# Performance work log

Hardware: AMD Instinct MI355X
Metric: run time of the kernel (lower is better)

## Reference

```python
import jax, jax.numpy as jnp
import numpy as np

N = 10000      # nodes
E = 320000     # edges (avg degree 32)
IN = 512       # in_channels
OUT = 128      # out_channels
H = 4          # in_head
C1 = 2 * OUT   # per-head hidden channels of conv1 (256)
NEG_SLOPE = 0.2


def setup_inputs() -> dict:
    key = jax.random.key(0)
    ks = jax.random.split(key, 12)
    x = jax.random.normal(ks[0], (N, IN), dtype=jnp.float32)
    edge_index = jax.random.randint(ks[1], (2, E), 0, N, dtype=jnp.int64)
    def glorot(k, shape):
        lim = np.sqrt(6.0 / (shape[0] + shape[-1])).astype(np.float32)
        return jax.random.uniform(k, shape, jnp.float32, -lim, lim)
    # conv1: GATv2Conv(IN -> C1 per head, heads=H)
    Wl1 = glorot(ks[2], (IN, H * C1))
    Wr1 = glorot(ks[3], (IN, H * C1))
    att1 = glorot(ks[4], (H, C1))
    b1 = jnp.zeros((H * C1,), jnp.float32)
    # conv2: GATv2Conv(H*C1 -> OUT, heads=1)
    Wl2 = glorot(ks[5], (H * C1, OUT))
    Wr2 = glorot(ks[6], (H * C1, OUT))
    att2 = glorot(ks[7], (1, OUT))
    b2 = jnp.zeros((OUT,), jnp.float32)
    return {"x": x, "edge_index": edge_index, "Wl1": Wl1, "Wr1": Wr1,
            "att1": att1, "b1": b1, "Wl2": Wl2, "Wr2": Wr2,
            "att2": att2, "b2": b2}


def gatv2_conv(x, src, dst, Wl, Wr, att, b, heads, ch):
    # x: [N, F_in]; src/dst: [E] (message src -> dst, softmax over dst)
    n = x.shape[0]
    xl = (x @ Wl).reshape(n, heads, ch)   # source-side projection
    xr = (x @ Wr).reshape(n, heads, ch)   # target-side projection
    # per-edge GATv2 score: att . LeakyReLU(xl_j + xr_i)   [E, H]
    e = jax.nn.leaky_relu(xl[src] + xr[dst], NEG_SLOPE)    # [E, H, C]
    s = jnp.einsum('ehc,hc->eh', e, att)                   # [E, H]
    # segment softmax over incoming edges of each dst node
    smax = jax.lax.stop_gradient(jax.ops.segment_max(s, dst, num_segments=n))
    ex = jnp.exp(s - smax[dst])
    denom = jax.ops.segment_sum(ex, dst, num_segments=n)
    alpha = ex / denom[dst]                                # [E, H]
    # weighted scatter-add of source messages
    out = jax.ops.segment_sum(alpha[:, :, None] * xl[src], dst, num_segments=n)
    return out.reshape(n, heads * ch) + b                  # concat heads + bias


def reference(x, edge_index, Wl1, Wr1, att1, b1, Wl2, Wr2, att2, b2):
    src, dst = edge_index[0], edge_index[1]
    h = gatv2_conv(x, src, dst, Wl1, Wr1, att1, b1, H, C1)
    h = jax.nn.relu(h)                                     # [N, H*C1]
    out = gatv2_conv(h, src, dst, Wl2, Wr2, att2, b2, 1, OUT)
    return out                                             # [N, OUT]
```

## Files before the change

kernel.cpp:

```cpp
#include <hip/hip_runtime.h>
#include <cfloat>

#define N_NODES 10000
#define N_EDGES 320000
#define IN_F    512
#define F1      1024
#define OUT_F   128
#define NEG     0.2f
#define BUCKET  128

typedef __attribute__((ext_vector_type(8))) short bf16x8;
typedef __attribute__((ext_vector_type(4))) float f32x4;
typedef __attribute__((ext_vector_type(2))) float f32x2;
typedef __attribute__((ext_vector_type(4))) unsigned int u32x4;

__device__ __forceinline__ float lrelu(float v) { return fmaxf(v, NEG * v); }

__device__ __forceinline__ unsigned short f2bf(float f) {
    unsigned u = __float_as_uint(f);
    u += 0x7fff + ((u >> 16) & 1);
    return (unsigned short)(u >> 16);
}
__device__ __forceinline__ float bf2f(unsigned short h) {
    return __uint_as_float(((unsigned)h) << 16);
}
__device__ __forceinline__ void u2f2(unsigned u, float& e0, float& e1) {
    e0 = __uint_as_float(u << 16);
    e1 = __uint_as_float(u & 0xffff0000u);
}

__device__ __forceinline__ float rsum16(float x) {
    x += __int_as_float(__builtin_amdgcn_update_dpp(0, __float_as_int(x), 0x121, 0xF, 0xF, false));
    x += __int_as_float(__builtin_amdgcn_update_dpp(0, __float_as_int(x), 0x122, 0xF, 0xF, false));
    x += __int_as_float(__builtin_amdgcn_update_dpp(0, __float_as_int(x), 0x124, 0xF, 0xF, false));
    x += __int_as_float(__builtin_amdgcn_update_dpp(0, __float_as_int(x), 0x128, 0xF, 0xF, false));
    return x;
}

__device__ __forceinline__ void gld_lds16(const void* g, void* l) {
    __builtin_amdgcn_global_load_lds(
        (const __attribute__((address_space(1))) unsigned int*)g,
        (__attribute__((address_space(3))) unsigned int*)l, 16, 0, 0);
}

#define PB_X  2500
#define PB_S  3750
#define PB_W1 4774
#define PB_END 5030

__device__ __forceinline__ void wt_body(const float* __restrict__ Wa,
                                        const float* __restrict__ Wb,
                                        unsigned short* __restrict__ tbf,
                                        int K, int NS, int n0, int k0, int t,
                                        float (*tile)[33]) {
    int j = t & 31;
    const float* W = (n0 < NS) ? Wa : Wb;
    int nb = (n0 < NS) ? n0 : n0 - NS;
#pragma unroll
    for (int r = 0; r < 4; ++r) {
        int kl = (t >> 5) + r * 8;
        tile[kl][j] = W[(size_t)(k0 + kl) * NS + nb + j];
    }
    __syncthreads();
#pragma unroll
    for (int r = 0; r < 4; ++r) {
        int nl = (t >> 5) + r * 8;
        tbf[(size_t)(n0 + nl) * K + k0 + j] = f2bf(tile[j][nl]);
    }
}

__global__ __launch_bounds__(256) void k_prep(const float* __restrict__ x,
                                              unsigned short* __restrict__ xbf,
                                              const int* __restrict__ ei,
                                              int* __restrict__ cnt,
                                              int* __restrict__ esrc,
                                              const float* __restrict__ Wl1,
                                              const float* __restrict__ Wr1,
                                              unsigned short* __restrict__ w1bf,
                                              const float* __restrict__ Wl2,
                                              const float* __restrict__ Wr2,
                                              unsigned short* __restrict__ w2bf) {
    __shared__ float tile[32][33];
    int bid = blockIdx.x, t = threadIdx.x;
    if (bid < PB_X) {
        int i = bid * 2048 + t * 8;
        f32x4 v0 = __builtin_nontemporal_load((const f32x4*)(x + i));
        f32x4 v1 = __builtin_nontemporal_load((const f32x4*)(x + i + 4));
        ushort4 h0, h1;
        h0.x = f2bf(v0.x); h0.y = f2bf(v0.y); h0.z = f2bf(v0.z); h0.w = f2bf(v0.w);
        h1.x = f2bf(v1.x); h1.y = f2bf(v1.y); h1.z = f2bf(v1.z); h1.w = f2bf(v1.w);
        *(ushort4*)(xbf + i) = h0;
        *(ushort4*)(xbf + i + 4) = h1;
    } else if (bid < PB_S) {
        int e = (bid - PB_X) * 256 + t;
        if (e < N_EDGES) {
            int d = ei[N_EDGES + e];
            int pos = atomicAdd(&cnt[d], 1);
            if (pos < BUCKET) esrc[(size_t)d * BUCKET + pos] = ei[e];
        }
    } else if (bid < PB_W1) {
        int local = bid - PB_S;
        wt_body(Wl1, Wr1, w1bf, IN_F, F1, (local & 63) * 32, (local >> 6) * 32, t, tile);
    } else {
        int local = bid - PB_W1;
        wt_body(Wl2, Wr2, w2bf, F1, OUT_F, (local & 7) * 32, (local >> 3) * 32, t, tile);
    }
}

template<int BM, int BN> struct GemmSmem {
    union {
        struct { short As[2 * BM * 32]; short Bs[2 * BN * 32]; } st;
        unsigned short ct[BM * (BN + 8)];
    };
};

template<int BM, int BN, int WR, int WC>
__global__ __launch_bounds__(256) void gemm_mfma(
        const unsigned short* __restrict__ A,
        const unsigned short* __restrict__ B,
        unsigned short* __restrict__ Cl, unsigned short* __restrict__ Cr,
        int M, int K, int NSPLIT, int ym,
        const int* __restrict__ cnt, int* __restrict__ esrc) {
    constexpr int NI = BM / (16 * WR);
    constexpr int NJ = BN / (16 * WC);
    __shared__ __align__(16) GemmSmem<BM, BN> sm;
    int t = threadIdx.x;
    int lane = t & 63, w = t >> 6;

    if ((int)blockIdx.y >= ym) {
        int nd = ((blockIdx.y - ym) * gridDim.x + blockIdx.x) * 4 + w;
        if (nd < N_NODES) {
            int deg = min(cnt[nd], 64);
            int p0 = nd * BUCKET;
            int v = (lane < deg) ? esrc[p0 + lane] : 0x7fffffff;
#pragma unroll
            for (int k = 2; k <= 64; k <<= 1) {
#pragma unroll
                for (int j = k >> 1; j > 0; j >>= 1) {
                    int other = __shfl_xor(v, j);
                    bool dir = ((lane & k) == 0);
                    bool lower = ((lane & j) == 0);
                    int mn = min(v, other), mx = max(v, other);
                    v = (lower == dir) ? mn : mx;
                }
            }
            if (lane < deg) esrc[p0 + lane] = v;
        }
        return;
    }

    int row0 = blockIdx.y * BM;
    int n0 = blockIdx.x * BN;
    int wr0 = (w / WC) * (NI * 16);
    int wc0 = (w % WC) * (NJ * 16);
    int q = lane >> 4, md = lane & 15;
    int srow = t >> 2;
    int skoff = (t & 3) * 8;

    f32x4 acc[NI][NJ];
#pragma unroll
    for (int i = 0; i < NI; ++i)
#pragma unroll
        for (int j = 0; j < NJ; ++j)
#pragma unroll
            for (int r = 0; r < 4; ++r) acc[i][j][r] = 0.f;

    for (int k0 = 0; k0 < K; k0 += 64) {
        __syncthreads();
#pragma unroll
        for (int pane = 0; pane < 2; ++pane)
#pragma unroll
            for (int is = 0; is < BM / 64; ++is) {
                int gr = row0 + is * 64 + srow;
                if (gr < M)
                    gld_lds16(A + (size_t)gr * K + k0 + pane * 32 + skoff,
                              &sm.st.As[pane * BM * 32 + (is * 64 + w * 16) * 32]);
            }
#pragma unroll
        for (int pane = 0; pane < 2; ++pane)
#pragma unroll
            for (int is = 0; is < BN / 64; ++is) {
                int gn = n0 + is * 64 + srow;
                gld_lds16(B + (size_t)gn * K + k0 + pane * 32 + skoff,
                          &sm.st.Bs[pane * BN * 32 + (is * 64 + w * 16) * 32]);
            }
        __syncthreads();

#pragma unroll
        for (int kk = 0; kk < 2; ++kk) {
            bf16x8 av[NI], bv[NJ];
#pragma unroll
            for (int i = 0; i < NI; ++i)
                av[i] = *(const bf16x8*)&sm.st.As[kk * BM * 32 + (wr0 + i * 16 + md) * 32 + q * 8];
#pragma unroll
            for (int j = 0; j < NJ; ++j)
                bv[j] = *(const bf16x8*)&sm.st.Bs[kk * BN * 32 + (wc0 + j * 16 + md) * 32 + q * 8];
#pragma unroll
            for (int i = 0; i < NI; ++i)
#pragma unroll
                for (int j = 0; j < NJ; ++j)
                    acc[i][j] = __builtin_amdgcn_mfma_f32_16x16x32_bf16(av[i], bv[j], acc[i][j], 0, 0, 0);
        }
    }

    __syncthreads();
#pragma unroll
    for (int i = 0; i < NI; ++i)
#pragma unroll
        for (int j = 0; j < NJ; ++j)
#pragma unroll
            for (int r = 0; r < 4; ++r)
                sm.ct[(wr0 + i * 16 + q * 4 + r) * (BN + 8) + wc0 + j * 16 + md] =
                    f2bf(acc[i][j][r]);
    __syncthreads();
    unsigned short* C = (n0 < NSPLIT) ? Cl : Cr;
    int cc0 = (n0 < NSPLIT) ? n0 : n0 - NSPLIT;
    constexpr int SEGS = BN / 8;
    for (int idx = t; idx < BM * SEGS; idx += 256) {
        int row = idx / SEGS, seg = idx % SEGS;
        if (row0 + row < M) {
            bf16x8 val = *(const bf16x8*)&sm.ct[row * (BN + 8) + seg * 8];
            *(bf16x8*)(C + (size_t)(row0 + row) * NSPLIT + cc0 + seg * 8) = val;
        }
    }
}

__global__ __launch_bounds__(256) void k_fused1(const unsigned short* __restrict__ xlbf,
                                                const unsigned short* __restrict__ xrbf,
                                                const int* __restrict__ cnt,
                                                const int* __restrict__ esrc,
                                                const float* __restrict__ att,
                                                const float* __restrict__ bias,
                                                unsigned short* __restrict__ hb) {
    int t = threadIdx.x;
    int w = t >> 6, lane = t & 63;
    int ni = w >> 1;
    int ww = w & 1;
    int nd = blockIdx.x * 2 + ni;
    int head = lane >> 4, sub = lane & 15;
    int ch = head * 256 + sub * 16;

    __shared__ float slx[4][4];
    __shared__ float4 sacc4[2][4][64];

    float4 r0, r1, r2, r3;
    {
        const u32x4* prx = (const u32x4*)(xrbf + (size_t)nd * F1 + ch);
        u32x4 xa = __builtin_nontemporal_load(prx);
        u32x4 xb = __builtin_nontemporal_load(prx + 1);
        u2f2(xa.x, r0.x, r0.y); u2f2(xa.y, r0.z, r0.w);
        u2f2(xa.z, r1.x, r1.y); u2f2(xa.w, r1.z, r1.w);
        u2f2(xb.x, r2.x, r2.y); u2f2(xb.y, r2.z, r2.w);
        u2f2(xb.z, r3.x, r3.y); u2f2(xb.w, r3.z, r3.w);
    }
    const float4* pa = (const float4*)(att + ch);
    float4 a0 = pa[0], a1 = pa[1], a2 = pa[2], a3 = pa[3];

    int deg = min(cnt[nd], BUCKET);
    int p0 = nd * BUCKET;
    int dege = min(deg, 64);
    int bkt = (lane < dege) ? esrc[p0 + lane] : 0;

    float l = 0.f;
    float4 acc0 = make_float4(0.f, 0.f, 0.f, 0.f);
    float4 acc1 = acc0, acc2 = acc0, acc3 = acc0;

    auto edge_body = [&](uint4 ca, uint4 cb) {
        float4 c0, c1, c2, c3;
        u2f2(ca.x, c0.x, c0.y); u2f2(ca.y, c0.z, c0.w);
        u2f2(ca.z, c1.x, c1.y); u2f2(ca.w, c1.z, c1.w);
        u2f2(cb.x, c2.x, c2.y); u2f2(cb.y, c2.z, c2.w);
        u2f2(cb.z, c3.x, c3.y); u2f2(cb.w, c3.z, c3.w);
        float u;
        float sl0, sa0, sl1, sa1, sl2, sa2, sl3, sa3;
        u = c0.x + r0.x; sl0 = a0.x * u;           sa0 = a0.x * fabsf(u);
        u = c0.y + r0.y; sl0 = fmaf(a0.y, u, sl0); sa0 = fmaf(a0.y, fabsf(u), sa0);
        u = c0.z + r0.z; sl0 = fmaf(a0.z, u, sl0); sa0 = fmaf(a0.z, fabsf(u), sa0);
        u = c0.w + r0.w; sl0 = fmaf(a0.w, u, sl0); sa0 = fmaf(a0.w, fabsf(u), sa0);
        u = c1.x + r1.x; sl1 = a1.x * u;           sa1 = a1.x * fabsf(u);
        u = c1.y + r1.y; sl1 = fmaf(a1.y, u, sl1); sa1 = fmaf(a1.y, fabsf(u), sa1);
        u = c1.z + r1.z; sl1 = fmaf(a1.z, u, sl1); sa1 = fmaf(a1.z, fabsf(u), sa1);
        u = c1.w + r1.w; sl1 = fmaf(a1.w, u, sl1); sa1 = fmaf(a1.w, fabsf(u), sa1);
        u = c2.x + r2.x; sl2 = a2.x * u;           sa2 = a2.x * fabsf(u);
        u = c2.y + r2.y; sl2 = fmaf(a2.y, u, sl2); sa2 = fmaf(a2.y, fabsf(u), sa2);
        u = c2.z + r2.z; sl2 = fmaf(a2.z, u, sl2); sa2 = fmaf(a2.z, fabsf(u), sa2);
        u = c2.w + r2.w; sl2 = fmaf(a2.w, u, sl2); sa2 = fmaf(a2.w, fabsf(u), sa2);
        u = c3.x + r3.x; sl3 = a3.x * u;           sa3 = a3.x * fabsf(u);
        u = c3.y + r3.y; sl3 = fmaf(a3.y, u, sl3); sa3 = fmaf(a3.y, fabsf(u), sa3);
        u = c3.z + r3.z; sl3 = fmaf(a3.z, u, sl3); sa3 = fmaf(a3.z, fabsf(u), sa3);
        u = c3.w + r3.w; sl3 = fmaf(a3.w, u, sl3); sa3 = fmaf(a3.w, fabsf(u), sa3);
        float sl = (sl0 + sl1) + (sl2 + sl3);
        float sa = (sa0 + sa1) + (sa2 + sa3);
        float s = rsum16(fmaf(0.6f, sl, 0.4f * sa));
        s = fminf(fmaxf(s, -60.f), 60.f);
        float al = __expf(s);
        l += al;
        acc0.x = fmaf(al, c0.x, acc0.x);
        acc0.y = fmaf(al, c0.y, acc0.y);
        acc0.z = fmaf(al, c0.z, acc0.z);
        acc0.w = fmaf(al, c0.w, acc0.w);
        acc1.x = fmaf(al, c1.x, acc1.x);
        acc1.y = fmaf(al, c1.y, acc1.y);
        acc1.z = fmaf(al, c1.z, acc1.z);
        acc1.w = fmaf(al, c1.w, acc1.w);
        acc2.x = fmaf(al, c2.x, acc2.x);
        acc2.y = fmaf(al, c2.y, acc2.y);
        acc2.z = fmaf(al, c2.z, acc2.z);
        acc2.w = fmaf(al, c2.w, acc2.w);
        acc3.x = fmaf(al, c3.x, acc3.x);
        acc3.y = fmaf(al, c3.y, acc3.y);
        acc3.z = fmaf(al, c3.z, acc3.z);
        acc3.w = fmaf(al, c3.w, acc3.w);
    };

    int idx = ww;
    uint4 ua, ub;
    if (idx < dege) {
        int sn = __shfl(bkt, idx);
        const uint4* pv = (const uint4*)(xlbf + (size_t)sn * F1 + ch);
        ua = pv[0]; ub = pv[1];
    }
    for (; idx < dege; idx += 2) {
        uint4 ca = ua, cb = ub;
        int nidx = idx + 2;
        if (nidx < dege) {
            int sn = __shfl(bkt, nidx);
            const uint4* pv = (const uint4*)(xlbf + (size_t)sn * F1 + ch);
            ua = pv[0]; ub = pv[1];
        }
        edge_body(ca, cb);
    }
    for (int p = p0 + 64 + ww; p < p0 + deg; p += 2) {
        const uint4* pv = (const uint4*)(xlbf + (size_t)esrc[p] * F1 + ch);
        edge_body(pv[0], pv[1]);
    }

    if (sub == 0) slx[w][head] = l;
    if (ww == 1) {
        sacc4[ni][0][lane] = acc0;
        sacc4[ni][1][lane] = acc1;
        sacc4[ni][2][lane] = acc2;
        sacc4[ni][3][lane] = acc3;
    }
    __syncthreads();
    if (ww == 0) {
        float L = l + slx[w ^ 1][head];
        float invL = (L > 0.f) ? 1.f / L : 0.f;
        const float4* pb = (const float4*)(bias + ch);
        size_t base = (size_t)nd * F1 + ch;
        float4 aa[4] = {acc0, acc1, acc2, acc3};
#pragma unroll
        for (int j = 0; j < 4; ++j) {
            float4 pt = sacc4[ni][j][lane];
            float4 b4 = pb[j];
            ushort4 hv;
            hv.x = f2bf(fmaxf(fmaf(aa[j].x + pt.x, invL, b4.x), 0.f));
            hv.y = f2bf(fmaxf(fmaf(aa[j].y + pt.y, invL, b4.y), 0.f));
            hv.z = f2bf(fmaxf(fmaf(aa[j].z + pt.z, invL, b4.z), 0.f));
            hv.w = f2bf(fmaxf(fmaf(aa[j].w + pt.w, invL, b4.w), 0.f));
            *(ushort4*)(hb + base + j * 4) = hv;
        }
    }
}

__global__ __launch_bounds__(256) void k_fused2(const unsigned short* __restrict__ xlbf,
                                                const unsigned short* __restrict__ xrbf,
                                                const int* __restrict__ cnt,
                                                const int* __restrict__ esrc,
                                                const float* __restrict__ att,
                                                const float* __restrict__ bias,
                                                float* __restrict__ out) {
    int t = threadIdx.x;
    int w = t >> 6, lane = t & 63;
    int nd = blockIdx.x * 4 + w;
    int g = lane >> 4, sub = lane & 15;
    int ch = sub * 8;

    __shared__ float slx2[4][4];
    __shared__ float sacc2[4][4][132];

    float r[8], a[8];
    {
        u32x4 u = __builtin_nontemporal_load(
            (const u32x4*)(xrbf + (size_t)nd * OUT_F + ch));
        u2f2(u.x, r[0], r[1]); u2f2(u.y, r[2], r[3]);
        u2f2(u.z, r[4], r[5]); u2f2(u.w, r[6], r[7]);
        float4 q0 = *(const float4*)(att + ch);
        float4 q1 = *(const float4*)(att + ch + 4);
        a[0] = q0.x; a[1] = q0.y; a[2] = q0.z; a[3] = q0.w;
        a[4] = q1.x; a[5] = q1.y; a[6] = q1.z; a[7] = q1.w;
    }
    int deg = min(cnt[nd], BUCKET);
    int p0 = nd * BUCKET;
    int p1 = p0 + deg;

    float l = 0.f;
    float acc[8] = {};
    uint4 cur, nxt;
    {
        int p = p0 + g;
        if (p < p1)     cur = *(const uint4*)(xlbf + (size_t)esrc[p] * OUT_F + ch);
        if (p + 4 < p1) nxt = *(const uint4*)(xlbf + (size_t)esrc[p + 4] * OUT_F + ch);
    }
    for (int p = p0 + g; p < p1; p += 4) {
        uint4 c = cur;
        cur = nxt;
        if (p + 8 < p1) nxt = *(const uint4*)(xlbf + (size_t)esrc[p + 8] * OUT_F + ch);
        float v[8];
        u2f2(c.x, v[0], v[1]); u2f2(c.y, v[2], v[3]);
        u2f2(c.z, v[4], v[5]); u2f2(c.w, v[6], v[7]);
        float uu;
        float slA, saA, slB, saB;
        uu = v[0] + r[0]; slA = a[0] * uu;           saA = a[0] * fabsf(uu);
        uu = v[1] + r[1]; slA = fmaf(a[1], uu, slA); saA = fmaf(a[1], fabsf(uu), saA);
        uu = v[2] + r[2]; slA = fmaf(a[2], uu, slA); saA = fmaf(a[2], fabsf(uu), saA);
        uu = v[3] + r[3]; slA = fmaf(a[3], uu, slA); saA = fmaf(a[3], fabsf(uu), saA);
        uu = v[4] + r[4]; slB = a[4] * uu;           saB = a[4] * fabsf(uu);
        uu = v[5] + r[5]; slB = fmaf(a[5], uu, slB); saB = fmaf(a[5], fabsf(uu), saB);
        uu = v[6] + r[6]; slB = fmaf(a[6], uu, slB); saB = fmaf(a[6], fabsf(uu), saB);
        uu = v[7] + r[7]; slB = fmaf(a[7], uu, slB); saB = fmaf(a[7], fabsf(uu), saB);
        float s = rsum16(fmaf(0.6f, slA + slB, 0.4f * (saA + saB)));
        s = fminf(fmaxf(s, -60.f), 60.f);
        float al = __expf(s);
        l += al;
#pragma unroll
        for (int k = 0; k < 8; ++k) acc[k] = fmaf(al, v[k], acc[k]);
    }

    if (sub == 0) slx2[w][g] = l;
    float4 v0 = make_float4(acc[0], acc[1], acc[2], acc[3]);
    float4 v1 = make_float4(acc[4], acc[5], acc[6], acc[7]);
    *(float4*)&sacc2[w][g][ch] = v0;
    *(float4*)&sacc2[w][g][ch + 4] = v1;
    __syncthreads();
    float L = slx2[w][0] + slx2[w][1] + slx2[w][2] + slx2[w][3];
    float invL = (L > 0.f) ? 1.f / L : 0.f;
    int c2 = lane * 2;
    float o0 = sacc2[w][0][c2] + sacc2[w][1][c2] + sacc2[w][2][c2] + sacc2[w][3][c2];
    float o1 = sacc2[w][0][c2 + 1] + sacc2[w][1][c2 + 1] + sacc2[w][2][c2 + 1] + sacc2[w][3][c2 + 1];
    float2 bf = *(const float2*)(bias + c2);
    f32x2 o;
    o.x = fmaf(o0, invL, bf.x);
    o.y = fmaf(o1, invL, bf.y);
    __builtin_nontemporal_store(o, (f32x2*)(out + (size_t)nd * OUT_F + c2));
}

extern "C" void kernel_launch(void* const* d_in, const int* in_sizes, int n_in,
                              void* d_out, int out_size, void* d_ws, size_t ws_size,
                              hipStream_t stream) {
    const float* x    = (const float*)d_in[0];
    const int*   ei   = (const int*)d_in[1];
    const float* Wl1  = (const float*)d_in[2];
    const float* Wr1  = (const float*)d_in[3];
    const float* att1 = (const float*)d_in[4];
    const float* b1   = (const float*)d_in[5];
    const float* Wl2  = (const float*)d_in[6];
    const float* Wr2  = (const float*)d_in[7];
    const float* att2 = (const float*)d_in[8];
    const float* b2   = (const float*)d_in[9];
    float* out = (float*)d_out;

    unsigned short* us = (unsigned short*)d_ws;
    unsigned short* xl1bf = us;
    unsigned short* xr1bf = xl1bf + (size_t)N_NODES * F1;
    unsigned short* xl2bf = xr1bf + (size_t)N_NODES * F1;
    unsigned short* xr2bf = xl2bf + (size_t)N_NODES * OUT_F;
    unsigned short* hb   = xr2bf + (size_t)N_NODES * OUT_F;
    unsigned short* xbf  = hb + (size_t)N_NODES * F1;
    unsigned short* w1bf = xbf + (size_t)N_NODES * IN_F;
    unsigned short* w2bf = w1bf + (size_t)2048 * IN_F;
    int* cnt   = (int*)(w2bf + (size_t)256 * F1);
    int* esrc  = cnt + (N_NODES + 16);

    hipMemsetAsync(cnt, 0, sizeof(int) * N_NODES, stream);
    k_prep<<<PB_END, 256, 0, stream>>>(x, xbf, ei, cnt, esrc,
                                       Wl1, Wr1, w1bf,
                                       Wl2, Wr2, w2bf);

    gemm_mfma<128, 128, 2, 2><<<dim3(16, 79 + 157), 256, 0, stream>>>(
        xbf, w1bf, xl1bf, xr1bf, N_NODES, IN_F, F1, 79, cnt, esrc);

    k_fused1<<<N_NODES / 2, 256, 0, stream>>>(xl1bf, xr1bf, cnt, esrc, att1, b1, hb);

    gemm_mfma<64, 64, 2, 2><<<dim3(4, 157), 256, 0, stream>>>(
        hb, w2bf, xl2bf, xr2bf, N_NODES, F1, OUT_F, 157, nullptr, nullptr);

    k_fused2<<<N_NODES / 4, 256, 0, stream>>>(xl2bf, xr2bf, cnt, esrc, att2, b2, out);
}
```

Baseline: 250.0 us.

## Double-buffer GEMM LDS tiles to overlap global loads with MFMA compute

Replaces the single-stage K-loop (load two 32-wide k panes, sync, compute) with a ping-pong LDS buffer over 32-wide k tiles. The next tile is prefetched into the alternate buffer while MFMAs run on the current one, with one waitcnt plus barrier per tile. This is meant to hide global-to-LDS latency behind compute. In exchange it takes twice as many iterations and barriers over K. The trailing __syncthreads before the epilogue is dropped and replaced by the final in-loop barrier, and the epilogue reuses that shared memory through a union.

```diff
diff --git a/kernel.cpp b/kernel.cpp
--- a/kernel.cpp
+++ b/kernel.cpp
@@ -109,7 +109,7 @@
 
 template<int BM, int BN> struct GemmSmem {
     union {
-        struct { short As[2 * BM * 32]; short Bs[2 * BN * 32]; } st;
+        struct { short As[2][BM * 32]; short Bs[2][BN * 32]; } st;
         unsigned short ct[BM * (BN + 8)];
     };
 };
@@ -165,45 +165,46 @@
 #pragma unroll
             for (int r = 0; r < 4; ++r) acc[i][j][r] = 0.f;
 
-    for (int k0 = 0; k0 < K; k0 += 64) {
-        __syncthreads();
-#pragma unroll
-        for (int pane = 0; pane < 2; ++pane)
-#pragma unroll
-            for (int is = 0; is < BM / 64; ++is) {
-                int gr = row0 + is * 64 + srow;
-                if (gr < M)
-                    gld_lds16(A + (size_t)gr * K + k0 + pane * 32 + skoff,
-                              &sm.st.As[pane * BM * 32 + (is * 64 + w * 16) * 32]);
-            }
-#pragma unroll
-        for (int pane = 0; pane < 2; ++pane)
-#pragma unroll
-            for (int is = 0; is < BN / 64; ++is) {
-                int gn = n0 + is * 64 + srow;
-                gld_lds16(B + (size_t)gn * K + k0 + pane * 32 + skoff,
-                          &sm.st.Bs[pane * BN * 32 + (is * 64 + w * 16) * 32]);
-            }
-        __syncthreads();
-
-#pragma unroll
-        for (int kk = 0; kk < 2; ++kk) {
-            bf16x8 av[NI], bv[NJ];
-#pragma unroll
-            for (int i = 0; i < NI; ++i)
-                av[i] = *(const bf16x8*)&sm.st.As[kk * BM * 32 + (wr0 + i * 16 + md) * 32 + q * 8];
+    auto STAGE = [&](int b, int k0) {
+#pragma unroll
+        for (int is = 0; is < BM / 64; ++is) {
+            int gr = row0 + is * 64 + srow;
+            if (gr < M)
+                gld_lds16(A + (size_t)gr * K + k0 + skoff,
+                          &sm.st.As[b][(is * 64 + w * 16) * 32]);
+        }
+#pragma unroll
+        for (int is = 0; is < BN / 64; ++is) {
+            int gn = n0 + is * 64 + srow;
+            gld_lds16(B + (size_t)gn * K + k0 + skoff,
+                      &sm.st.Bs[b][(is * 64 + w * 16) * 32]);
+        }
+    };
+
+    int nt = K >> 5;
+    STAGE(0, 0);
+    asm volatile("s_waitcnt vmcnt(0)" ::: "memory");
+    __builtin_amdgcn_s_barrier();
+    int cur = 0;
+    for (int ti = 0; ti < nt; ++ti) {
+        if (ti + 1 < nt) STAGE(cur ^ 1, (ti + 1) << 5);
+        bf16x8 av[NI], bv[NJ];
+#pragma unroll
+        for (int i = 0; i < NI; ++i)
+            av[i] = *(const bf16x8*)&sm.st.As[cur][(wr0 + i * 16 + md) * 32 + q * 8];
+#pragma unroll
+        for (int j = 0; j < NJ; ++j)
+            bv[j] = *(const bf16x8*)&sm.st.Bs[cur][(wc0 + j * 16 + md) * 32 + q * 8];
+#pragma unroll
+        for (int i = 0; i < NI; ++i)
 #pragma unroll
             for (int j = 0; j < NJ; ++j)
-                bv[j] = *(const bf16x8*)&sm.st.Bs[kk * BN * 32 + (wc0 + j * 16 + md) * 32 + q * 8];
-#pragma unroll
-            for (int i = 0; i < NI; ++i)
-#pragma unroll
-                for (int j = 0; j < NJ; ++j)
-                    acc[i][j] = __builtin_amdgcn_mfma_f32_16x16x32_bf16(av[i], bv[j], acc[i][j], 0, 0, 0);
-        }
-    }
-
-    __syncthreads();
+                acc[i][j] = __builtin_amdgcn_mfma_f32_16x16x32_bf16(av[i], bv[j], acc[i][j], 0, 0, 0);
+        asm volatile("s_waitcnt vmcnt(0)" ::: "memory");
+        __builtin_amdgcn_s_barrier();
+        cur ^= 1;
+    }
+
 #pragma unroll
     for (int i = 0; i < NI; ++i)
 #pragma unroll
```

Result: no change. 253.5 us (+1.4%).
